# Kernel tuning notes

Measured on AMD Instinct MI355X. Metric: run time of the kernel, lower is better.

The kernel has to match this reference:

```python
import jax, jax.numpy as jnp
import numpy as np

E = 200_000   # edges (messages)
T = 2_000_000 # triplets
N = 20_000    # atoms/nodes
H = 128       # hidden_channels
INT = 64      # int_emb_size
BAS = 8       # basis_emb_size
OUT_EMB = 256 # out_emb_channels
NRAD = 6
SBF_DIM = 7 * 6  # num_spherical * num_radial = 42
NB = 4        # num_blocks
OUTC = 1      # num_targets


def setup_inputs() -> dict:
    key = jax.random.key(0)
    ks = iter(jax.random.split(key, 64))

    def w(shape):
        # glorot-ish scaled weights, stored as [in, out] for x @ W
        return jax.random.normal(next(ks), shape, jnp.float32) / np.sqrt(shape[-2])

    return dict(
        x=jax.random.normal(next(ks), (E, H), jnp.float32),
        rbf=jax.random.normal(next(ks), (E, NRAD), jnp.float32),
        sbf=jax.random.normal(next(ks), (T, SBF_DIM), jnp.float32),
        # interaction block params, stacked over NB blocks
        W_rbf1=w((NB, NRAD, BAS)), W_rbf2=w((NB, BAS, H)),
        W_sbf1=w((NB, SBF_DIM, BAS)), W_sbf2=w((NB, BAS, INT)),
        W_kj=w((NB, H, H)), b_kj=jnp.zeros((NB, H), jnp.float32),
        W_ji=w((NB, H, H)), b_ji=jnp.zeros((NB, H), jnp.float32),
        W_down=w((NB, H, INT)), W_up=w((NB, INT, H)),
        Wb=w((NB, 2, H, H)), bb=jnp.zeros((NB, 2, H), jnp.float32),   # num_before_skip=1 -> 2 linears
        Wa=w((NB, 4, H, H)), ba=jnp.zeros((NB, 4, H), jnp.float32),   # num_after_skip=2 -> 4 linears
        W_lin=w((NB, H, H)), b_lin=jnp.zeros((NB, H), jnp.float32),
        # output block params, stacked over NB+1 blocks
        Wo_rbf=w((NB + 1, NRAD, H)),
        Wo_up=w((NB + 1, H, OUT_EMB)), bo_up=jnp.zeros((NB + 1, OUT_EMB), jnp.float32),
        Wo_lins=w((NB + 1, 3, OUT_EMB, OUT_EMB)), bo_lins=jnp.zeros((NB + 1, 3, OUT_EMB), jnp.float32),
        Wo_out=w((NB + 1, OUT_EMB, OUTC)),
        idx_kj=jax.random.randint(next(ks), (T,), 0, E, jnp.int32),
        idx_ji=jax.random.randint(next(ks), (T,), 0, E, jnp.int32),
        idx_i=jax.random.randint(next(ks), (E,), 0, N, jnp.int32),
        num_nodes=N,
    )


def _interaction(b, x, rbf, sbf, idx_kj, idx_ji, p):
    act = jax.nn.silu
    x_ji = act(x @ p['W_ji'][b] + p['b_ji'][b])
    x_kj = act(x @ p['W_kj'][b] + p['b_kj'][b])
    rbf_t = (rbf @ p['W_rbf1'][b]) @ p['W_rbf2'][b]          # [E,H]
    x_kj = act((x_kj * rbf_t) @ p['W_down'][b])              # [E,INT]
    sbf_t = (sbf @ p['W_sbf1'][b]) @ p['W_sbf2'][b]          # [T,INT]
    m = x_kj[idx_kj] * sbf_t                                  # triplet gather [T,INT]
    agg = jax.ops.segment_sum(m, idx_ji, num_segments=x.shape[0])  # scatter-add [E,INT]
    x_kj = act(agg @ p['W_up'][b])                            # [E,H]
    h = x_ji + x_kj
    # residual layers before skip (1 layer = 2 linears)
    h = h + act(act(h @ p['Wb'][b, 0] + p['bb'][b, 0]) @ p['Wb'][b, 1] + p['bb'][b, 1])
    h = act(h @ p['W_lin'][b] + p['b_lin'][b]) + x
    # residual layers after skip (2 layers = 4 linears)
    for l in range(2):
        h = h + act(act(h @ p['Wa'][b, 2 * l] + p['ba'][b, 2 * l]) @ p['Wa'][b, 2 * l + 1] + p['ba'][b, 2 * l + 1])
    return h


def _output(b, x, rbf, idx_i, num_nodes, p):
    act = jax.nn.silu
    t = (rbf @ p['Wo_rbf'][b]) * x                            # [E,H]
    t = jax.ops.segment_sum(t, idx_i, num_segments=num_nodes) # [N,H]
    t = t @ p['Wo_up'][b] + p['bo_up'][b]
    for l in range(3):
        t = act(t @ p['Wo_lins'][b, l] + p['bo_lins'][b, l])
    return t @ p['Wo_out'][b]                                 # [N,OUTC]


def reference(x, rbf, sbf, W_rbf1, W_rbf2, W_sbf1, W_sbf2, W_kj, b_kj, W_ji, b_ji,
              W_down, W_up, Wb, bb, Wa, ba, W_lin, b_lin,
              Wo_rbf, Wo_up, bo_up, Wo_lins, bo_lins, Wo_out,
              idx_kj, idx_ji, idx_i, num_nodes):
    p = dict(W_rbf1=W_rbf1, W_rbf2=W_rbf2, W_sbf1=W_sbf1, W_sbf2=W_sbf2,
             W_kj=W_kj, b_kj=b_kj, W_ji=W_ji, b_ji=b_ji, W_down=W_down, W_up=W_up,
             Wb=Wb, bb=bb, Wa=Wa, ba=ba, W_lin=W_lin, b_lin=b_lin,
             Wo_rbf=Wo_rbf, Wo_up=Wo_up, bo_up=bo_up,
             Wo_lins=Wo_lins, bo_lins=bo_lins, Wo_out=Wo_out)
    P = _output(0, x, rbf, idx_i, num_nodes, p)
    for b in range(NB):  # fixed small layer loop
        x = _interaction(b, x, rbf, sbf, idx_kj, idx_ji, p)
        P = P + _output(b + 1, x, rbf, idx_i, num_nodes, p)
    return P
```

## Files before the change

### kernel.cpp

```cpp
#include <hip/hip_runtime.h>
#include <hip/hip_bf16.h>

#define E_EDGES 200000
#define T_TRIP  2000000
#define N_NODES 20000
#define H_DIM   128
#define INT_DIM 64
#define BAS     8
#define OUT_EMB 256
#define NRAD    6
#define SBF_D   42
#define NB      4

#define F_BIAS 1
#define F_SILU 2
#define F_RES  4
#define F_GATE 8

typedef __attribute__((ext_vector_type(8))) __bf16 bf16x8;
typedef __attribute__((ext_vector_type(4))) float f32x4;
typedef unsigned short u16;

__device__ __forceinline__ float silu_f(float v) { return v / (1.0f + __expf(-v)); }

__device__ __forceinline__ u16 f2bf(float f) {
    unsigned int u = __float_as_uint(f);
    u += 0x7FFF + ((u >> 16) & 1);
    return (u16)(u >> 16);
}
__device__ __forceinline__ float bf2f(u16 h) {
    return __uint_as_float(((unsigned int)h) << 16);
}

__device__ __forceinline__ void st_split(char* H, char* L, int row, int col, int stride, float v) {
    u16 hh = f2bf(v);
    u16 ll = f2bf(v - bf2f(hh));
    int off = (row * stride + col * 2) ^ ((row & 7) << 4);
    *reinterpret_cast<u16*>(H + off) = hh;
    *reinterpret_cast<u16*>(L + off) = ll;
}
__device__ __forceinline__ float ld_split(const char* H, const char* L, int row, int col, int stride) {
    int off = (row * stride + col * 2) ^ ((row & 7) << 4);
    return bf2f(*reinterpret_cast<const u16*>(H + off))
         + bf2f(*reinterpret_cast<const u16*>(L + off));
}

struct BF8x4 { bf16x8 h[4]; bf16x8 l[4]; };

__device__ __forceinline__ BF8x4 loadB128f(const u16* __restrict__ Bh, const u16* __restrict__ Bl,
                                           int k0, int wn, int l15, int khalf)
{
    BF8x4 f;
    #pragma unroll
    for (int n = 0; n < 4; ++n) {
        size_t bo = (size_t)(wn * 64 + n * 16 + l15) * 128 + k0 + khalf;
        f.h[n] = *reinterpret_cast<const bf16x8*>(Bh + bo);
        f.l[n] = *reinterpret_cast<const bf16x8*>(Bl + bo);
    }
    return f;
}
__device__ __forceinline__ BF8x4 loadB64f(const u16* __restrict__ Bh, const u16* __restrict__ Bl,
                                          int k0, int wn, int l15, int khalf)
{
    BF8x4 f;
    #pragma unroll
    for (int n = 0; n < 4; ++n) {
        size_t bo = (size_t)(wn * 64 + n * 16 + l15) * 64 + k0 + khalf;
        f.h[n] = *reinterpret_cast<const bf16x8*>(Bh + bo);
        f.l[n] = *reinterpret_cast<const bf16x8*>(Bl + bo);
    }
    return f;
}

__device__ __forceinline__ void mfma_cluster(
    const char* AH, const char* AL, int k0, int wm, int l15, int khalf,
    const BF8x4& b, f32x4 acc[2][4])
{
    #pragma unroll
    for (int m = 0; m < 2; ++m) {
        int row = wm * 32 + m * 16 + l15;
        int off = (row * 256 + (k0 + khalf) * 2) ^ ((row & 7) << 4);
        bf16x8 ah = *reinterpret_cast<const bf16x8*>(AH + off);
        bf16x8 al = *reinterpret_cast<const bf16x8*>(AL + off);
        #pragma unroll
        for (int n = 0; n < 4; ++n) {
            acc[m][n] = __builtin_amdgcn_mfma_f32_16x16x32_bf16(ah, b.h[n], acc[m][n], 0, 0, 0);
            acc[m][n] = __builtin_amdgcn_mfma_f32_16x16x32_bf16(al, b.h[n], acc[m][n], 0, 0, 0);
            acc[m][n] = __builtin_amdgcn_mfma_f32_16x16x32_bf16(ah, b.l[n], acc[m][n], 0, 0, 0);
        }
    }
}
__device__ __forceinline__ void mfma_cluster64(
    const char* AH, const char* AL, int k0, int wm, int l15, int khalf,
    const BF8x4& b, f32x4 acc[2][4])
{
    #pragma unroll
    for (int m = 0; m < 2; ++m) {
        int row = wm * 32 + m * 16 + l15;
        int off = (row * 128 + (k0 + khalf) * 2) ^ ((row & 7) << 4);
        bf16x8 ah = *reinterpret_cast<const bf16x8*>(AH + off);
        bf16x8 al = *reinterpret_cast<const bf16x8*>(AL + off);
        #pragma unroll
        for (int n = 0; n < 4; ++n) {
            acc[m][n] = __builtin_amdgcn_mfma_f32_16x16x32_bf16(ah, b.h[n], acc[m][n], 0, 0, 0);
            acc[m][n] = __builtin_amdgcn_mfma_f32_16x16x32_bf16(al, b.h[n], acc[m][n], 0, 0, 0);
            acc[m][n] = __builtin_amdgcn_mfma_f32_16x16x32_bf16(ah, b.l[n], acc[m][n], 0, 0, 0);
        }
    }
}

__device__ __forceinline__ void mm128_pipe(
    const char* AH, const char* AL,
    const u16* __restrict__ Bh, const u16* __restrict__ Bl, BF8x4& pre,
    const u16* __restrict__ nBh, const u16* __restrict__ nBl,
    int wm, int wn, int l15, int khalf, f32x4 acc[2][4])
{
    BF8x4 c0 = pre;
    BF8x4 c1 = loadB128f(Bh, Bl, 32, wn, l15, khalf);
    mfma_cluster(AH, AL, 0, wm, l15, khalf, c0, acc);
    BF8x4 c2 = loadB128f(Bh, Bl, 64, wn, l15, khalf);
    mfma_cluster(AH, AL, 32, wm, l15, khalf, c1, acc);
    BF8x4 c3 = loadB128f(Bh, Bl, 96, wn, l15, khalf);
    mfma_cluster(AH, AL, 64, wm, l15, khalf, c2, acc);
    if (nBh) pre = loadB128f(nBh, nBl, 0, wn, l15, khalf);
    mfma_cluster(AH, AL, 96, wm, l15, khalf, c3, acc);
}
__device__ __forceinline__ void mm64_pipe(
    const char* AH, const char* AL,
    const u16* __restrict__ Bh, const u16* __restrict__ Bl, BF8x4& pre,
    const u16* __restrict__ nBh, const u16* __restrict__ nBl,
    int wm, int wn, int l15, int khalf, f32x4 acc[2][4])
{
    BF8x4 c0 = pre;
    BF8x4 c1 = loadB64f(Bh, Bl, 32, wn, l15, khalf);
    mfma_cluster64(AH, AL, 0, wm, l15, khalf, c0, acc);
    if (nBh) pre = loadB128f(nBh, nBl, 0, wn, l15, khalf);
    mfma_cluster64(AH, AL, 32, wm, l15, khalf, c1, acc);
}

__global__ __launch_bounds__(256) void wprep(
    const float* __restrict__ src, u16* __restrict__ hi,
    u16* __restrict__ lo, int K, int N)
{
    int e = blockIdx.x * 256 + threadIdx.x;
    int total = K * N;
    if (e >= total) return;
    size_t base = (size_t)blockIdx.y * total;
    float a = src[base + e];
    int k = e / N, n = e - k * N;
    u16 h = f2bf(a);
    u16 l = f2bf(a - bf2f(h));
    hi[base + (size_t)n * K + k] = h;
    lo[base + (size_t)n * K + k] = l;
}

__global__ __launch_bounds__(256) void mfma_gemm(
    const float* __restrict__ A,
    const u16* __restrict__ Bhi, const u16* __restrict__ Blo,
    const float* __restrict__ bias, const float* __restrict__ res,
    const float* __restrict__ rbf8v, const float* __restrict__ Wr2,
    float* __restrict__ C, int M, int N, int K, int flags)
{
    __shared__ u16 AsH[128 * 32];
    __shared__ u16 AsL[128 * 32];

    const int tid  = threadIdx.x;
    const int lane = tid & 63;
    const int w    = tid >> 6;
    const int wm   = w >> 1, wn = w & 1;
    const int bm   = blockIdx.y * 128;
    const int bn   = blockIdx.x * 64;
    const int l15  = lane & 15;
    const int khalf = (lane >> 4) * 8;

    const int sr = tid >> 1;
    const int sc = (tid & 1) * 16;
    int grow = bm + sr; if (grow >= M) grow = M - 1;
    const float* gA = &A[(size_t)grow * K + sc];

    int bcol[2];
    #pragma unroll
    for (int n = 0; n < 2; ++n) bcol[n] = bn + wn * 32 + n * 16 + l15;

    f32x4 acc[4][2] = {};

    for (int k0 = 0; k0 < K; k0 += 32) {
        __syncthreads();
        {
            const float* p = gA + k0;
            float4 f0 = *reinterpret_cast<const float4*>(p);
            float4 f1 = *reinterpret_cast<const float4*>(p + 4);
            float4 f2 = *reinterpret_cast<const float4*>(p + 8);
            float4 f3 = *reinterpret_cast<const float4*>(p + 12);
            float vv[16] = {f0.x,f0.y,f0.z,f0.w, f1.x,f1.y,f1.z,f1.w,
                            f2.x,f2.y,f2.z,f2.w, f3.x,f3.y,f3.z,f3.w};
            const int swz = (sr & 7) << 4;
            #pragma unroll
            for (int q = 0; q < 4; ++q) {
                u16 h[4], l[4];
                #pragma unroll
                for (int j = 0; j < 4; ++j) {
                    float a = vv[q * 4 + j];
                    h[j] = f2bf(a);
                    l[j] = f2bf(a - bf2f(h[j]));
                }
                int off = (sr * 64 + (sc / 4 + q) * 8) ^ swz;
                *reinterpret_cast<ushort4*>((char*)AsH + off) = make_ushort4(h[0], h[1], h[2], h[3]);
                *reinterpret_cast<ushort4*>((char*)AsL + off) = make_ushort4(l[0], l[1], l[2], l[3]);
            }
        }
        __syncthreads();

        bf16x8 bh[2], bl[2];
        #pragma unroll
        for (int n = 0; n < 2; ++n) {
            size_t bo = (size_t)bcol[n] * K + k0 + khalf;
            bh[n] = *reinterpret_cast<const bf16x8*>(Bhi + bo);
            bl[n] = *reinterpret_cast<const bf16x8*>(Blo + bo);
        }

        #pragma unroll
        for (int m = 0; m < 4; ++m) {
            int ri  = wm * 64 + m * 16 + l15;
            int off = (ri * 64 + khalf * 2) ^ ((ri & 7) << 4);
            bf16x8 ah = *reinterpret_cast<const bf16x8*>((const char*)AsH + off);
            bf16x8 al = *reinterpret_cast<const bf16x8*>((const char*)AsL + off);
            #pragma unroll
            for (int n = 0; n < 2; ++n) {
                acc[m][n] = __builtin_amdgcn_mfma_f32_16x16x32_bf16(ah, bh[n], acc[m][n], 0, 0, 0);
                acc[m][n] = __builtin_amdgcn_mfma_f32_16x16x32_bf16(al, bh[n], acc[m][n], 0, 0, 0);
                acc[m][n] = __builtin_amdgcn_mfma_f32_16x16x32_bf16(ah, bl[n], acc[m][n], 0, 0, 0);
            }
        }
    }

    const int r4 = (lane >> 4) * 4;
    #pragma unroll
    for (int m = 0; m < 4; ++m) {
        #pragma unroll
        for (int r = 0; r < 4; ++r) {
            int row = bm + wm * 64 + m * 16 + r4 + r;
            if (row >= M) continue;
            #pragma unroll
            for (int n = 0; n < 2; ++n) {
                int col = bn + wn * 32 + n * 16 + l15;
                float v = acc[m][n][r];
                if (flags & F_BIAS) v += bias[col];
                if (flags & F_SILU) v = silu_f(v);
                if (flags & F_GATE) {
                    float g = 0.f;
                    #pragma unroll
                    for (int j = 0; j < 8; ++j)
                        g = fmaf(rbf8v[(size_t)row * 8 + j], Wr2[j * N + col], g);
                    v *= g;
                }
                if (flags & F_RES) v += res[(size_t)row * N + col];
                C[(size_t)row * N + col] = v;
            }
        }
    }
}

__global__ __launch_bounds__(256, 2) void pre_fuse(
    const float* __restrict__ X, const float* __restrict__ R8,
    const u16* __restrict__ Wjih, const u16* __restrict__ Wjil, const float* __restrict__ bji,
    const u16* __restrict__ Wkjh, const u16* __restrict__ Wkjl, const float* __restrict__ bkj,
    const float* __restrict__ Wr2,
    const u16* __restrict__ Wdnh, const u16* __restrict__ Wdnl,
    float* __restrict__ E1, float* __restrict__ C1)
{
    __shared__ u16 XH[64 * 128], XL[64 * 128];
    __shared__ u16 IH[64 * 128], IL[64 * 128];

    const int tid  = threadIdx.x;
    const int lane = tid & 63;
    const int w    = tid >> 6;
    const int wm   = w >> 1, wn = w & 1;
    const int bm   = blockIdx.x * 64;
    const int l15  = lane & 15;
    const int khalf = (lane >> 4) * 8;
    const int r4   = (lane >> 4) * 4;

    BF8x4 pre = loadB128f(Wjih, Wjil, 0, wn, l15, khalf);

    {
        int r  = tid >> 2;
        int c0 = (tid & 3) * 32;
        const float* p = &X[(size_t)(bm + r) * H_DIM + c0];
        const int swz = (r & 7) << 4;
        #pragma unroll
        for (int q = 0; q < 8; ++q) {
            float4 f = *reinterpret_cast<const float4*>(p + q * 4);
            float vv[4] = {f.x, f.y, f.z, f.w};
            u16 h[4], l[4];
            #pragma unroll
            for (int j = 0; j < 4; ++j) {
                h[j] = f2bf(vv[j]);
                l[j] = f2bf(vv[j] - bf2f(h[j]));
            }
            int off = (r * 256 + c0 * 2 + q * 8) ^ swz;
            *reinterpret_cast<ushort4*>((char*)XH + off) = make_ushort4(h[0], h[1], h[2], h[3]);
            *reinterpret_cast<ushort4*>((char*)XL + off) = make_ushort4(l[0], l[1], l[2], l[3]);
        }
    }
    __syncthreads();

    {
        f32x4 acc[2][4] = {};
        mm128_pipe((char*)XH, (char*)XL, Wjih, Wjil, pre, Wkjh, Wkjl,
                   wm, wn, l15, khalf, acc);
        #pragma unroll
        for (int n = 0; n < 4; ++n) {
            int col = wn * 64 + n * 16 + l15;
            float bv = bji[col];
            #pragma unroll
            for (int m = 0; m < 2; ++m)
                #pragma unroll
                for (int r = 0; r < 4; ++r) {
                    int row = wm * 32 + m * 16 + r4 + r;
                    E1[(size_t)(bm + row) * H_DIM + col] = silu_f(acc[m][n][r] + bv);
                }
        }
    }
    {
        f32x4 acc[2][4] = {};
        mm128_pipe((char*)XH, (char*)XL, Wkjh, Wkjl, pre, nullptr, nullptr,
                   wm, wn, l15, khalf, acc);
        #pragma unroll
        for (int n = 0; n < 4; ++n) {
            int col = wn * 64 + n * 16 + l15;
            float bv = bkj[col];
            #pragma unroll
            for (int m = 0; m < 2; ++m)
                #pragma unroll
                for (int r = 0; r < 4; ++r) {
                    int row = wm * 32 + m * 16 + r4 + r;
                    float v = silu_f(acc[m][n][r] + bv);
                    float g = 0.f;
                    #pragma unroll
                    for (int j = 0; j < 8; ++j)
                        g = fmaf(R8[(size_t)(bm + row) * 8 + j], Wr2[j * H_DIM + col], g);
                    st_split((char*)IH, (char*)IL, row, col, 256, v * g);
                }
        }
    }
    __syncthreads();

    {
        f32x4 acc[2][2] = {};
        #pragma unroll
        for (int k0 = 0; k0 < 128; k0 += 32) {
            bf16x8 bh[2], bl[2];
            #pragma unroll
            for (int n = 0; n < 2; ++n) {
                size_t bo = (size_t)(wn * 32 + n * 16 + l15) * 128 + k0 + khalf;
                bh[n] = *reinterpret_cast<const bf16x8*>(Wdnh + bo);
                bl[n] = *reinterpret_cast<const bf16x8*>(Wdnl + bo);
            }
            #pragma unroll
            for (int m = 0; m < 2; ++m) {
                int row = wm * 32 + m * 16 + l15;
                int off = (row * 256 + (k0 + khalf) * 2) ^ ((row & 7) << 4);
                bf16x8 ah = *reinterpret_cast<const bf16x8*>((const char*)IH + off);
                bf16x8 al = *reinterpret_cast<const bf16x8*>((const char*)IL + off);
                #pragma unroll
                for (int n = 0; n < 2; ++n) {
                    acc[m][n] = __builtin_amdgcn_mfma_f32_16x16x32_bf16(ah, bh[n], acc[m][n], 0, 0, 0);
                    acc[m][n] = __builtin_amdgcn_mfma_f32_16x16x32_bf16(al, bh[n], acc[m][n], 0, 0, 0);
                    acc[m][n] = __builtin_amdgcn_mfma_f32_16x16x32_bf16(ah, bl[n], acc[m][n], 0, 0, 0);
                }
            }
        }
        #pragma unroll
        for (int n = 0; n < 2; ++n) {
            int col = wn * 32 + n * 16 + l15;
            #pragma unroll
            for (int m = 0; m < 2; ++m)
                #pragma unroll
                for (int r = 0; r < 4; ++r) {
                    int row = wm * 32 + m * 16 + r4 + r;
                    C1[(size_t)(bm + row) * INT_DIM + col] = silu_f(acc[m][n][r]);
                }
        }
    }
}

struct ChainP {
    const u16 *uph, *upl;
    const u16 *b0h, *b0l, *b1h, *b1l;
    const u16 *lnh, *lnl;
    const u16 *a0h, *a0l, *a1h, *a1l, *a2h, *a2l, *a3h, *a3l;
    const float *bb0, *bb1, *blin, *ba0, *ba1, *ba2, *ba3;
};

__global__ __launch_bounds__(256, 2) void post_chain(
    const float* __restrict__ AGG, const float* __restrict__ E1,
    const float* __restrict__ X, ChainP p, float* __restrict__ OUT)
{
    __shared__ u16 GH[64 * 64],  GL[64 * 64];
    __shared__ u16 P0H[64 * 128], P0L[64 * 128];
    __shared__ u16 P1H[64 * 128], P1L[64 * 128];

    const int tid  = threadIdx.x;
    const int lane = tid & 63;
    const int w    = tid >> 6;
    const int wm   = w >> 1, wn = w & 1;
    const int bm   = blockIdx.x * 64;
    const int l15  = lane & 15;
    const int khalf = (lane >> 4) * 8;
    const int r4   = (lane >> 4) * 4;

    BF8x4 pre = loadB64f(p.uph, p.upl, 0, wn, l15, khalf);

    {
        int r  = tid >> 2;
        int c0 = (tid & 3) * 16;
        const float* pg = &AGG[(size_t)(bm + r) * INT_DIM + c0];
        const int swz = (r & 7) << 4;
        #pragma unroll
        for (int q = 0; q < 4; ++q) {
            float4 f = *reinterpret_cast<const float4*>(pg + q * 4);
            float vv[4] = {f.x, f.y, f.z, f.w};
            u16 h[4], l[4];
            #pragma unroll
            for (int j = 0; j < 4; ++j) {
                h[j] = f2bf(vv[j]);
                l[j] = f2bf(vv[j] - bf2f(h[j]));
            }
            int off = (r * 128 + c0 * 2 + q * 8) ^ swz;
            *reinterpret_cast<ushort4*>((char*)GH + off) = make_ushort4(h[0], h[1], h[2], h[3]);
            *reinterpret_cast<ushort4*>((char*)GL + off) = make_ushort4(l[0], l[1], l[2], l[3]);
        }
    }
    __syncthreads();

    f32x4 acc[2][4];

    #pragma unroll
    for (int m = 0; m < 2; ++m)
        #pragma unroll
        for (int n = 0; n < 4; ++n) acc[m][n] = f32x4{0.f, 0.f, 0.f, 0.f};
    mm64_pipe((char*)GH, (char*)GL, p.uph, p.upl, pre, p.b0h, p.b0l,
              wm, wn, l15, khalf, acc);
    #pragma unroll
    for (int n = 0; n < 4; ++n) {
        int col = wn * 64 + n * 16 + l15;
        #pragma unroll
        for (int m = 0; m < 2; ++m)
            #pragma unroll
            for (int r = 0; r < 4; ++r) {
                int row = wm * 32 + m * 16 + r4 + r;
                float v = E1[(size_t)(bm + row) * H_DIM + col] + silu_f(acc[m][n][r]);
                st_split((char*)P0H, (char*)P0L, row, col, 256, v);
            }
// ... 25 lines not shown
    }

    #define STAGE_RES(SRC_H, SRC_L, WH, WL, BIAS, RES_H, RES_L, NWH, NWL)               \
    {                                                                                   \
        _Pragma("unroll")                                                               \
        for (int m = 0; m < 2; ++m)                                                     \
            _Pragma("unroll")                                                           \
            for (int n = 0; n < 4; ++n) acc[m][n] = f32x4{0.f, 0.f, 0.f, 0.f};          \
        mm128_pipe((char*)SRC_H, (char*)SRC_L, WH, WL, pre, NWH, NWL,                   \
                   wm, wn, l15, khalf, acc);                                            \
        _Pragma("unroll")                                                               \
        for (int n = 0; n < 4; ++n) {                                                   \
            int col = wn * 64 + n * 16 + l15;                                           \
            float bv = BIAS[col];                                                       \
            _Pragma("unroll")                                                           \
            for (int m = 0; m < 2; ++m)                                                 \
                _Pragma("unroll")                                                       \
                for (int r = 0; r < 4; ++r) {                                           \
                    int row = wm * 32 + m * 16 + r4 + r;                                \
                    float v = ld_split((char*)RES_H, (char*)RES_L, row, col, 256)       \
                            + silu_f(acc[m][n][r] + bv);                                \
                    st_split((char*)RES_H, (char*)RES_L, row, col, 256, v);             \
                }                                                                       \
        }                                                                               \
        __syncthreads();                                                                \
    }

    STAGE_PLAIN(P0H, P0L, p.b0h, p.b0l, p.bb0, P1H, P1L, p.b1h, p.b1l)
    STAGE_RES(P1H, P1L, p.b1h, p.b1l, p.bb1, P0H, P0L, p.lnh, p.lnl)

    {
        #pragma unroll
        for (int m = 0; m < 2; ++m)
            #pragma unroll
            for (int n = 0; n < 4; ++n) acc[m][n] = f32x4{0.f, 0.f, 0.f, 0.f};
        mm128_pipe((char*)P0H, (char*)P0L, p.lnh, p.lnl, pre, p.a0h, p.a0l,
                   wm, wn, l15, khalf, acc);
        #pragma unroll
        for (int n = 0; n < 4; ++n) {
            int col = wn * 64 + n * 16 + l15;
            float bv = p.blin[col];
            #pragma unroll
            for (int m = 0; m < 2; ++m)
                #pragma unroll
                for (int r = 0; r < 4; ++r) {
                    int row = wm * 32 + m * 16 + r4 + r;
                    float v = silu_f(acc[m][n][r] + bv) + X[(size_t)(bm + row) * H_DIM + col];
                    st_split((char*)P1H, (char*)P1L, row, col, 256, v);
                }
        }
        __syncthreads();
    }

    STAGE_PLAIN(P1H, P1L, p.a0h, p.a0l, p.ba0, P0H, P0L, p.a1h, p.a1l)
    STAGE_RES(P0H, P0L, p.a1h, p.a1l, p.ba1, P1H, P1L, p.a2h, p.a2l)
    STAGE_PLAIN(P1H, P1L, p.a2h, p.a2l, p.ba2, P0H, P0L, p.a3h, p.a3l)

    {
        #pragma unroll
        for (int m = 0; m < 2; ++m)
            #pragma unroll
            for (int n = 0; n < 4; ++n) acc[m][n] = f32x4{0.f, 0.f, 0.f, 0.f};
        mm128_pipe((char*)P0H, (char*)P0L, p.a3h, p.a3l, pre, nullptr, nullptr,
                   wm, wn, l15, khalf, acc);
        #pragma unroll
        for (int n = 0; n < 4; ++n) {
            int col = wn * 64 + n * 16 + l15;
            float bv = p.ba3[col];
            #pragma unroll
            for (int m = 0; m < 2; ++m)
                #pragma unroll
                for (int r = 0; r < 4; ++r) {
                    int row = wm * 32 + m * 16 + r4 + r;
                    float v = ld_split((char*)P1H, (char*)P1L, row, col, 256)
                            + silu_f(acc[m][n][r] + bv);
                    OUT[(size_t)(bm + row) * H_DIM + col] = v;
                }
        }
    }
    #undef STAGE_PLAIN
    #undef STAGE_RES
}

__global__ __launch_bounds__(256) void rbf8_kernel(
    const float* __restrict__ rbf, const float* __restrict__ W1,
    float* __restrict__ r8, int Ecount)
{
    int e = blockIdx.x * blockDim.x + threadIdx.x;
    if (e >= Ecount) return;
    float rv[NRAD];
    #pragma unroll
    for (int k = 0; k < NRAD; ++k) rv[k] = rbf[(size_t)e * NRAD + k];
    float acc[BAS] = {};
    #pragma unroll
    for (int k = 0; k < NRAD; ++k)
        #pragma unroll
        for (int j = 0; j < BAS; ++j)
            acc[j] = fmaf(rv[k], W1[k * BAS + j], acc[j]);
    float4* o = reinterpret_cast<float4*>(&r8[(size_t)e * BAS]);
    o[0] = make_float4(acc[0], acc[1], acc[2], acc[3]);
    o[1] = make_float4(acc[4], acc[5], acc[6], acc[7]);
}

__global__ __launch_bounds__(256) void csr_count(
    const int* __restrict__ idx, int* __restrict__ cnt, int n)
{
    int i = blockIdx.x * 256 + threadIdx.x;
    if (i < n) atomicAdd(&cnt[idx[i]], 1);
}

__global__ __launch_bounds__(256) void scan_block(
    const int* __restrict__ cnt, int* __restrict__ ptr, int* __restrict__ bsum, int n)
{
    __shared__ int s[256];
    int i = blockIdx.x * 256 + threadIdx.x;
    int v = (i < n) ? cnt[i] : 0;
    s[threadIdx.x] = v;
    __syncthreads();
    #pragma unroll
    for (int off = 1; off < 256; off <<= 1) {
        int t = (threadIdx.x >= off) ? s[threadIdx.x - off] : 0;
        __syncthreads();
        s[threadIdx.x] += t;
        __syncthreads();
    }
    if (i < n) ptr[i] = s[threadIdx.x] - v;
    if (threadIdx.x == 255) bsum[blockIdx.x] = s[255];
}

__global__ __launch_bounds__(1024) void scan_aux(int* __restrict__ bsum, int nb)
{
    __shared__ int s[1024];
    int v = (threadIdx.x < nb) ? bsum[threadIdx.x] : 0;
    s[threadIdx.x] = v;
    __syncthreads();
    #pragma unroll
    for (int off = 1; off < 1024; off <<= 1) {
        int t = (threadIdx.x >= off) ? s[threadIdx.x - off] : 0;
        __syncthreads();
        s[threadIdx.x] += t;
        __syncthreads();
    }
    if (threadIdx.x < nb) bsum[threadIdx.x] = s[threadIdx.x] - v;
}

__global__ __launch_bounds__(256) void scan_add(
    int* __restrict__ ptr, const int* __restrict__ bsum, int n)
{
    int i = blockIdx.x * 256 + threadIdx.x;
    if (i < n) ptr[i] += bsum[blockIdx.x];
}

__global__ __launch_bounds__(256) void csr_fill(
    const int* __restrict__ idx, int* __restrict__ cursor,
    int* __restrict__ perm, int n)
{
    int i = blockIdx.x * 256 + threadIdx.x;
    if (i >= n) return;
    int pos = atomicAdd(&cursor[idx[i]], 1);
    perm[pos] = i;
}

__global__ __launch_bounds__(256) void permute_s8(
    const float* __restrict__ sbf, const float* __restrict__ W1all,
    const int* __restrict__ idx_kj, const int* __restrict__ tperm,
    u16* __restrict__ ps8, int* __restrict__ pkj, int Tcount)
// ... 30 lines not shown
        *reinterpret_cast<ushort4*>(op) = o0;
        *reinterpret_cast<ushort4*>(op + 4) = o1;
    }
}

__device__ __forceinline__ float dot8_bf(uint4 r, const float* w2) {
    float s;
    s  = bf2f((u16)(r.x)) * w2[0] + bf2f((u16)(r.x >> 16)) * w2[1];
    s += bf2f((u16)(r.y)) * w2[2] + bf2f((u16)(r.y >> 16)) * w2[3];
    s += bf2f((u16)(r.z)) * w2[4] + bf2f((u16)(r.z >> 16)) * w2[5];
    s += bf2f((u16)(r.w)) * w2[6] + bf2f((u16)(r.w >> 16)) * w2[7];
    return s;
}

__global__ __launch_bounds__(256) void triplet_gather2(
    const u16* __restrict__ ps8b, const float* __restrict__ Wsb2,
    const float* __restrict__ xkj, const int* __restrict__ pkj,
    const int* __restrict__ tptr, const int* __restrict__ tcnt,
    float* __restrict__ agg, int Ecount)
{
    const int lane = threadIdx.x & 63;
    int wid = (blockIdx.x * blockDim.x + threadIdx.x) >> 6;
    const int nw = (gridDim.x * blockDim.x) >> 6;
    float w2[BAS];
    #pragma unroll
    for (int j = 0; j < BAS; ++j) w2[j] = Wsb2[j * INT_DIM + lane];

    for (int e = wid; e < Ecount; e += nw) {
        int start = tptr[e];
        int end   = start + tcnt[e];
        float acc0 = 0.f, acc1 = 0.f;
        int i = start;
        for (; i + 1 < end; i += 2) {
            uint4 ra = *reinterpret_cast<const uint4*>(&ps8b[(size_t)i * BAS]);
            uint4 rb = *reinterpret_cast<const uint4*>(&ps8b[(size_t)(i + 1) * BAS]);
            int e0 = pkj[i], e1 = pkj[i + 1];
            float s0 = dot8_bf(ra, w2);
            float s1 = dot8_bf(rb, w2);
            acc0 = fmaf(xkj[(size_t)e0 * INT_DIM + lane], s0, acc0);
            acc1 = fmaf(xkj[(size_t)e1 * INT_DIM + lane], s1, acc1);
        }
        if (i < end) {
            uint4 ra = *reinterpret_cast<const uint4*>(&ps8b[(size_t)i * BAS]);
            int e0 = pkj[i];
            acc0 = fmaf(xkj[(size_t)e0 * INT_DIM + lane], dot8_bf(ra, w2), acc0);
        }
        agg[(size_t)e * INT_DIM + lane] = acc0 + acc1;
    }
}

__global__ __launch_bounds__(256) void out_gather(
    const float* __restrict__ rbf, const float* __restrict__ Wor,
    const float* __restrict__ x,
    const int* __restrict__ eptr, const int* __restrict__ ecnt,
    const int* __restrict__ eperm, float* __restrict__ tN, int Nn)
{
    const int lane = threadIdx.x & 63;
    int wid = (blockIdx.x * blockDim.x + threadIdx.x) >> 6;
    const int nw = (gridDim.x * blockDim.x) >> 6;
    float wr0[NRAD], wr1[NRAD];
    #pragma unroll
    for (int k = 0; k < NRAD; ++k) {
        wr0[k] = Wor[k * H_DIM + lane];
        wr1[k] = Wor[k * H_DIM + lane + 64];
    }
    for (int n = wid; n < Nn; n += nw) {
        int start = eptr[n];
        int end   = start + ecnt[n];
        float a0 = 0.f, a1 = 0.f;
        for (int i = start; i < end; ++i) {
            int e = eperm[i];
            const float2* rp = reinterpret_cast<const float2*>(&rbf[(size_t)e * NRAD]);
            float2 r0 = rp[0], r1 = rp[1], r2 = rp[2];
            float rA = r0.x*wr0[0] + r0.y*wr0[1] + r1.x*wr0[2]
                     + r1.y*wr0[3] + r2.x*wr0[4] + r2.y*wr0[5];
            float rB = r0.x*wr1[0] + r0.y*wr1[1] + r1.x*wr1[2]
                     + r1.y*wr1[3] + r2.x*wr1[4] + r2.y*wr1[5];
            a0 = fmaf(rA, x[(size_t)e * H_DIM + lane], a0);
            a1 = fmaf(rB, x[(size_t)e * H_DIM + lane + 64], a1);
        }
        tN[(size_t)n * H_DIM + lane] = a0;
        tN[(size_t)n * H_DIM + lane + 64] = a1;
    }
}

__global__ __launch_bounds__(256) void out_final(
    const float* __restrict__ Tb, const float* __restrict__ Wo,
    float* __restrict__ P, int Nn)
{
    const int lane = threadIdx.x & 63;
    int node = (blockIdx.x * blockDim.x + threadIdx.x) >> 6;
    if (node >= Nn) return;
    float s = 0.f;
    #pragma unroll
    for (int i = 0; i < 4; ++i) {
        int c = lane + i * 64;
        s = fmaf(Tb[(size_t)node * OUT_EMB + c], Wo[c], s);
    }
    #pragma unroll
    for (int o = 32; o > 0; o >>= 1) s += __shfl_xor(s, o);
    if (lane == 0) P[node] += s;
}

extern "C" void kernel_launch(void* const* d_in, const int* in_sizes, int n_in,
                              void* d_out, int out_size, void* d_ws, size_t ws_size,
                              hipStream_t stream)
{
    const float* x_in    = (const float*)d_in[0];
    const float* rbf     = (const float*)d_in[1];
    const float* sbf     = (const float*)d_in[2];
    const float* W_rbf1  = (const float*)d_in[3];
    const float* W_rbf2  = (const float*)d_in[4];
    const float* W_sbf1  = (const float*)d_in[5];
    const float* W_sbf2  = (const float*)d_in[6];
    const float* W_kj    = (const float*)d_in[7];
    const float* b_kj    = (const float*)d_in[8];
    const float* W_ji    = (const float*)d_in[9];
    const float* b_ji    = (const float*)d_in[10];
    const float* W_down  = (const float*)d_in[11];
    const float* W_up    = (const float*)d_in[12];
    const float* Wb      = (const float*)d_in[13];
    const float* bb      = (const float*)d_in[14];
    const float* Wa      = (const float*)d_in[15];
    const float* ba      = (const float*)d_in[16];
    const float* W_lin   = (const float*)d_in[17];
    const float* b_lin   = (const float*)d_in[18];
    const float* Wo_rbf  = (const float*)d_in[19];
    const float* Wo_up   = (const float*)d_in[20];
    const float* bo_up   = (const float*)d_in[21];
    const float* Wo_lins = (const float*)d_in[22];
    const float* bo_lins = (const float*)d_in[23];
    const float* Wo_out  = (const float*)d_in[24];
    const int*   idx_kj  = (const int*)d_in[25];
    const int*   idx_ji  = (const int*)d_in[26];
    const int*   idx_i   = (const int*)d_in[27];

    char* ws = (char*)d_ws;
    size_t off = 0;
    auto alloc = [&](size_t bytes) -> void* {
        void* p = (void*)(ws + off);
        off += (bytes + 255) & ~(size_t)255;
        return p;
    };
    float* XA = (float*)alloc((size_t)E_EDGES * H_DIM * 4);
    float* XB = (float*)alloc((size_t)E_EDGES * H_DIM * 4);
    float* E1 = (float*)alloc((size_t)E_EDGES * H_DIM * 4);
    float* C1 = (float*)alloc((size_t)E_EDGES * INT_DIM * 4);
    float* C2 = (float*)alloc((size_t)E_EDGES * INT_DIM * 4);
    float* R8 = (float*)alloc((size_t)E_EDGES * BAS * 4);
    float* TN = (float*)alloc((size_t)N_NODES * H_DIM * 4);
    float* T1 = (float*)alloc((size_t)N_NODES * OUT_EMB * 4);
    float* T2 = (float*)alloc((size_t)N_NODES * OUT_EMB * 4);
    u16* HKJ = (u16*)alloc(4  * 16384 * 2); u16* LKJ = (u16*)alloc(4  * 16384 * 2);
    u16* HJI = (u16*)alloc(4  * 16384 * 2); u16* LJI = (u16*)alloc(4  * 16384 * 2);
    u16* HDN = (u16*)alloc(4  * 8192  * 2); u16* LDN = (u16*)alloc(4  * 8192  * 2);
    u16* HUP = (u16*)alloc(4  * 8192  * 2); u16* LUP = (u16*)alloc(4  * 8192  * 2);
    u16* HWB = (u16*)alloc(8  * 16384 * 2); u16* LWB = (u16*)alloc(8  * 16384 * 2);
    u16* HWA = (u16*)alloc(16 * 16384 * 2); u16* LWA = (u16*)alloc(16 * 16384 * 2);
    u16* HLN = (u16*)alloc(4  * 16384 * 2); u16* LLN = (u16*)alloc(4  * 16384 * 2);
    u16* HOU = (u16*)alloc(5  * 32768 * 2); u16* LOU = (u16*)alloc(5  * 32768 * 2);
    u16* HOL = (u16*)alloc(15 * 65536 * 2); u16* LOL = (u16*)alloc(15 * 65536 * 2);
    int* tcnt  = (int*)alloc((size_t)E_EDGES * 4);
    int* tptr  = (int*)alloc((size_t)E_EDGES * 4);
    int* tcur  = (int*)alloc((size_t)E_EDGES * 4);
    int* tperm = (int*)alloc((size_t)T_TRIP * 4);
    int* tbsum = (int*)alloc(1024 * 4);
    int* ecnt  = (int*)alloc((size_t)N_NODES * 4);
    int* eptr  = (int*)alloc((size_t)N_NODES * 4);
    int* ecur  = (int*)alloc((size_t)N_NODES * 4);
    int* eperm = (int*)alloc((size_t)E_EDGES * 4);
    int* ebsum = (int*)alloc(1024 * 4);
    u16* PS8 = (u16*)alloc((size_t)NB * T_TRIP * BAS * 2);
    int* PKJ = (int*)alloc((size_t)T_TRIP * 4);
    (void)ws_size;

    auto prep = [&](const float* src, u16* hi, u16* lo, int K, int N, int cnt) {
        dim3 g((K * N + 255) / 256, cnt);
        hipLaunchKernelGGL(wprep, g, dim3(256), 0, stream, src, hi, lo, K, N);
    };
    prep(W_kj,    HKJ, LKJ, 128, 128, 4);
    prep(W_ji,    HJI, LJI, 128, 128, 4);
    prep(W_down,  HDN, LDN, 128, 64,  4);
    prep(W_up,    HUP, LUP, 64,  128, 4);
    prep(Wb,      HWB, LWB, 128, 128, 8);
    prep(Wa,      HWA, LWA, 128, 128, 16);
    prep(W_lin,   HLN, LLN, 128, 128, 4);
    prep(Wo_up,   HOU, LOU, 128, 256, 5);
    prep(Wo_lins, HOL, LOL, 256, 256, 15);

    {
        const int nbT = (E_EDGES + 255) / 256;
        hipMemsetAsync(tcnt, 0, (size_t)E_EDGES * 4, stream);
        hipLaunchKernelGGL(csr_count, dim3((T_TRIP + 255) / 256), dim3(256), 0, stream,
                           idx_ji, tcnt, T_TRIP);
        hipLaunchKernelGGL(scan_block, dim3(nbT), dim3(256), 0, stream, tcnt, tptr, tbsum, E_EDGES);
        hipLaunchKernelGGL(scan_aux, dim3(1), dim3(1024), 0, stream, tbsum, nbT);
        hipLaunchKernelGGL(scan_add, dim3(nbT), dim3(256), 0, stream, tptr, tbsum, E_EDGES);
        hipMemcpyAsync(tcur, tptr, (size_t)E_EDGES * 4, hipMemcpyDeviceToDevice, stream);
        hipLaunchKernelGGL(csr_fill, dim3((T_TRIP + 255) / 256), dim3(256), 0, stream,
                           idx_ji, tcur, tperm, T_TRIP);
    }
    {
        const int nbN = (N_NODES + 255) / 256;
        hipMemsetAsync(ecnt, 0, (size_t)N_NODES * 4, stream);
        hipLaunchKernelGGL(csr_count, dim3((E_EDGES + 255) / 256), dim3(256), 0, stream,
                           idx_i, ecnt, E_EDGES);
        hipLaunchKernelGGL(scan_block, dim3(nbN), dim3(256), 0, stream, ecnt, eptr, ebsum, N_NODES);
        hipLaunchKernelGGL(scan_aux, dim3(1), dim3(1024), 0, stream, ebsum, nbN);
        hipLaunchKernelGGL(scan_add, dim3(nbN), dim3(256), 0, stream, eptr, ebsum, N_NODES);
        hipMemcpyAsync(ecur, eptr, (size_t)N_NODES * 4, hipMemcpyDeviceToDevice, stream);
        hipLaunchKernelGGL(csr_fill, dim3((E_EDGES + 255) / 256), dim3(256), 0, stream,
                           idx_i, ecur, eperm, E_EDGES);
    }
    hipLaunchKernelGGL(permute_s8, dim3((T_TRIP + 255) / 256), dim3(256), 0, stream,
                       sbf, W_sbf1, idx_kj, tperm, PS8, PKJ, T_TRIP);

    auto gemm = [&](const float* A, const u16* Bh, const u16* Bl, const float* bias,
                    const float* res, const float* r8, const float* Wr2f,
                    float* C, int M, int N, int K, int flags) {
        dim3 g(N / 64, (M + 127) / 128), b(256);
        hipLaunchKernelGGL(mfma_gemm, g, b, 0, stream,
                           A, Bh, Bl, bias, res, r8, Wr2f, C, M, N, K, flags);
    };

    float* P = (float*)d_out;
    hipMemsetAsync(P, 0, (size_t)N_NODES * sizeof(float), stream);

    auto out_block = [&](int ob, const float* xcur) {
        hipLaunchKernelGGL(out_gather, dim3(2048), dim3(256), 0, stream,
                           rbf, Wo_rbf + (size_t)ob * NRAD * H_DIM, xcur,
                           eptr, ecnt, eperm, TN, N_NODES);
        gemm(TN, HOU + (size_t)ob * 32768, LOU + (size_t)ob * 32768,
             bo_up + (size_t)ob * OUT_EMB, nullptr, nullptr, nullptr,
             T1, N_NODES, OUT_EMB, H_DIM, F_BIAS);
        float* src = T1; float* dst = T2;
        for (int l = 0; l < 3; ++l) {
            gemm(src, HOL + (size_t)(ob * 3 + l) * 65536, LOL + (size_t)(ob * 3 + l) * 65536,
                 bo_lins + (size_t)(ob * 3 + l) * OUT_EMB, nullptr, nullptr, nullptr,
                 dst, N_NODES, OUT_EMB, OUT_EMB, F_BIAS | F_SILU);
            float* tmp = src; src = dst; dst = tmp;
        }
        hipLaunchKernelGGL(out_final, dim3((N_NODES * 64 + 255) / 256), dim3(256), 0, stream,
                           src, Wo_out + (size_t)ob * OUT_EMB, P, N_NODES);
    };

    out_block(0, x_in);

    const float* xcur = x_in;
    const int EB = E_EDGES / 64;
    for (int b = 0; b < NB; ++b) {
        float* xnext = (b % 2 == 0) ? XB : XA;
        hipLaunchKernelGGL(rbf8_kernel, dim3((E_EDGES + 255) / 256), dim3(256), 0, stream,
                           rbf, W_rbf1 + (size_t)b * NRAD * BAS, R8, E_EDGES);
        hipLaunchKernelGGL(pre_fuse, dim3(EB), dim3(256), 0, stream,
                           xcur, R8,
                           HJI + (size_t)b * 16384, LJI + (size_t)b * 16384, b_ji + (size_t)b * H_DIM,
                           HKJ + (size_t)b * 16384, LKJ + (size_t)b * 16384, b_kj + (size_t)b * H_DIM,
                           W_rbf2 + (size_t)b * BAS * H_DIM,
                           HDN + (size_t)b * 8192, LDN + (size_t)b * 8192,
                           E1, C1);
        hipLaunchKernelGGL(triplet_gather2, dim3(2048), dim3(256), 0, stream,
                           PS8 + (size_t)b * T_TRIP * BAS, W_sbf2 + (size_t)b * BAS * INT_DIM,
                           C1, PKJ, tptr, tcnt, C2, E_EDGES);
        ChainP cp;
        cp.uph = HUP + (size_t)b * 8192;  cp.upl = LUP + (size_t)b * 8192;
        cp.b0h = HWB + (size_t)(b * 2 + 0) * 16384; cp.b0l = LWB + (size_t)(b * 2 + 0) * 16384;
        cp.b1h = HWB + (size_t)(b * 2 + 1) * 16384; cp.b1l = LWB + (size_t)(b * 2 + 1) * 16384;
        cp.lnh = HLN + (size_t)b * 16384; cp.lnl = LLN + (size_t)b * 16384;
        cp.a0h = HWA + (size_t)(b * 4 + 0) * 16384; cp.a0l = LWA + (size_t)(b * 4 + 0) * 16384;
        cp.a1h = HWA + (size_t)(b * 4 + 1) * 16384; cp.a1l = LWA + (size_t)(b * 4 + 1) * 16384;
        cp.a2h = HWA + (size_t)(b * 4 + 2) * 16384; cp.a2l = LWA + (size_t)(b * 4 + 2) * 16384;
        cp.a3h = HWA + (size_t)(b * 4 + 3) * 16384; cp.a3l = LWA + (size_t)(b * 4 + 3) * 16384;
        cp.bb0 = bb + (size_t)(b * 2 + 0) * H_DIM;
        cp.bb1 = bb + (size_t)(b * 2 + 1) * H_DIM;
        cp.blin = b_lin + (size_t)b * H_DIM;
        cp.ba0 = ba + (size_t)(b * 4 + 0) * H_DIM;
        cp.ba1 = ba + (size_t)(b * 4 + 1) * H_DIM;
        cp.ba2 = ba + (size_t)(b * 4 + 2) * H_DIM;
        cp.ba3 = ba + (size_t)(b * 4 + 3) * H_DIM;
        hipLaunchKernelGGL(post_chain, dim3(EB), dim3(256), 0, stream,
                           C2, E1, xcur, cp, xnext);
        xcur = xnext;
        out_block(b + 1, xcur);
    }
}
```

Baseline: 4.618 ms.

## Fuse output-block MLP chain into one kernel with LDS-resident intermediates

Replaces the four separate GEMM launches and the final reduction of each output block with a single out_chain kernel. Each block keeps 32 node rows resident in shared memory as split bf16 hi/lo values across the up-projection, three SiLU linears and the final dot product. This removes the global round-trips of the N×256 intermediates and several launches. It also wraps the MFMA clusters in s_setprio to raise wave priority during matrix math. The cost is large LDS use per block, which limits occupancy, and each block re-reads the full weight matrices from global memory or cache.

Measured after the change: 4.438 ms. -3.9%, faster.

```diff
diff --git a/kernel.cpp b/kernel.cpp
--- a/kernel.cpp
+++ b/kernel.cpp
@@ -12,11 +12,6 @@
 #define SBF_D   42
 #define NB      4
 
-#define F_BIAS 1
-#define F_SILU 2
-#define F_RES  4
-#define F_GATE 8
-
 typedef __attribute__((ext_vector_type(8))) __bf16 bf16x8;
 typedef __attribute__((ext_vector_type(4))) float f32x4;
 typedef unsigned short u16;
@@ -71,11 +66,24 @@
     }
     return f;
 }
+__device__ __forceinline__ BF8x4 loadB256f(const u16* __restrict__ Bh, const u16* __restrict__ Bl,
+                                           int k0, int wn, int l15, int khalf)
+{
+    BF8x4 f;
+    #pragma unroll
+    for (int n = 0; n < 4; ++n) {
+        size_t bo = (size_t)(wn * 64 + n * 16 + l15) * 256 + k0 + khalf;
+        f.h[n] = *reinterpret_cast<const bf16x8*>(Bh + bo);
+        f.l[n] = *reinterpret_cast<const bf16x8*>(Bl + bo);
+    }
+    return f;
+}
 
 __device__ __forceinline__ void mfma_cluster(
     const char* AH, const char* AL, int k0, int wm, int l15, int khalf,
     const BF8x4& b, f32x4 acc[2][4])
 {
+    __builtin_amdgcn_s_setprio(1);
     #pragma unroll
     for (int m = 0; m < 2; ++m) {
         int row = wm * 32 + m * 16 + l15;
@@ -89,11 +97,13 @@
             acc[m][n] = __builtin_amdgcn_mfma_f32_16x16x32_bf16(ah, b.l[n], acc[m][n], 0, 0, 0);
         }
     }
+    __builtin_amdgcn_s_setprio(0);
 }
 __device__ __forceinline__ void mfma_cluster64(
     const char* AH, const char* AL, int k0, int wm, int l15, int khalf,
     const BF8x4& b, f32x4 acc[2][4])
 {
+    __builtin_amdgcn_s_setprio(1);
     #pragma unroll
     for (int m = 0; m < 2; ++m) {
         int row = wm * 32 + m * 16 + l15;
@@ -107,6 +117,27 @@
             acc[m][n] = __builtin_amdgcn_mfma_f32_16x16x32_bf16(ah, b.l[n], acc[m][n], 0, 0, 0);
         }
     }
+    __builtin_amdgcn_s_setprio(0);
+}
+__device__ __forceinline__ void mfma_cluster512(
+    const char* AH, const char* AL, int k0, int l15, int khalf,
+    const BF8x4& b, f32x4 acc[2][4])
+{
+    __builtin_amdgcn_s_setprio(1);
+    #pragma unroll
+    for (int m = 0; m < 2; ++m) {
+        int row = m * 16 + l15;
+        int off = (row * 512 + (k0 + khalf) * 2) ^ ((row & 7) << 4);
+        bf16x8 ah = *reinterpret_cast<const bf16x8*>(AH + off);
+        bf16x8 al = *reinterpret_cast<const bf16x8*>(AL + off);
+        #pragma unroll
+        for (int n = 0; n < 4; ++n) {
+            acc[m][n] = __builtin_amdgcn_mfma_f32_16x16x32_bf16(ah, b.h[n], acc[m][n], 0, 0, 0);
+            acc[m][n] = __builtin_amdgcn_mfma_f32_16x16x32_bf16(al, b.h[n], acc[m][n], 0, 0, 0);
+            acc[m][n] = __builtin_amdgcn_mfma_f32_16x16x32_bf16(ah, b.l[n], acc[m][n], 0, 0, 0);
+        }
+    }
+    __builtin_amdgcn_s_setprio(0);
 }
 
 __device__ __forceinline__ void mm128_pipe(
@@ -152,113 +183,6 @@
     u16 l = f2bf(a - bf2f(h));
     hi[base + (size_t)n * K + k] = h;
     lo[base + (size_t)n * K + k] = l;
-}
-
-__global__ __launch_bounds__(256) void mfma_gemm(
-    const float* __restrict__ A,
-    const u16* __restrict__ Bhi, const u16* __restrict__ Blo,
-    const float* __restrict__ bias, const float* __restrict__ res,
-    const float* __restrict__ rbf8v, const float* __restrict__ Wr2,
-    float* __restrict__ C, int M, int N, int K, int flags)
-{
-    __shared__ u16 AsH[128 * 32];
-    __shared__ u16 AsL[128 * 32];
-
-    const int tid  = threadIdx.x;
-    const int lane = tid & 63;
-    const int w    = tid >> 6;
-    const int wm   = w >> 1, wn = w & 1;
-    const int bm   = blockIdx.y * 128;
-    const int bn   = blockIdx.x * 64;
-    const int l15  = lane & 15;
-    const int khalf = (lane >> 4) * 8;
-
-    const int sr = tid >> 1;
-    const int sc = (tid & 1) * 16;
-    int grow = bm + sr; if (grow >= M) grow = M - 1;
-    const float* gA = &A[(size_t)grow * K + sc];
-
-    int bcol[2];
-    #pragma unroll
-    for (int n = 0; n < 2; ++n) bcol[n] = bn + wn * 32 + n * 16 + l15;
-
-    f32x4 acc[4][2] = {};
-
-    for (int k0 = 0; k0 < K; k0 += 32) {
-        __syncthreads();
-        {
-            const float* p = gA + k0;
-            float4 f0 = *reinterpret_cast<const float4*>(p);
-            float4 f1 = *reinterpret_cast<const float4*>(p + 4);
-            float4 f2 = *reinterpret_cast<const float4*>(p + 8);
-            float4 f3 = *reinterpret_cast<const float4*>(p + 12);
-            float vv[16] = {f0.x,f0.y,f0.z,f0.w, f1.x,f1.y,f1.z,f1.w,
-                            f2.x,f2.y,f2.z,f2.w, f3.x,f3.y,f3.z,f3.w};
-            const int swz = (sr & 7) << 4;
-            #pragma unroll
-            for (int q = 0; q < 4; ++q) {
-                u16 h[4], l[4];
-                #pragma unroll
-                for (int j = 0; j < 4; ++j) {
-                    float a = vv[q * 4 + j];
-                    h[j] = f2bf(a);
-                    l[j] = f2bf(a - bf2f(h[j]));
-                }
-                int off = (sr * 64 + (sc / 4 + q) * 8) ^ swz;
-                *reinterpret_cast<ushort4*>((char*)AsH + off) = make_ushort4(h[0], h[1], h[2], h[3]);
-                *reinterpret_cast<ushort4*>((char*)AsL + off) = make_ushort4(l[0], l[1], l[2], l[3]);
-            }
-        }
-        __syncthreads();
-
-        bf16x8 bh[2], bl[2];
-        #pragma unroll
-        for (int n = 0; n < 2; ++n) {
-            size_t bo = (size_t)bcol[n] * K + k0 + khalf;
-            bh[n] = *reinterpret_cast<const bf16x8*>(Bhi + bo);
-            bl[n] = *reinterpret_cast<const bf16x8*>(Blo + bo);
-        }
-
-        #pragma unroll
-        for (int m = 0; m < 4; ++m) {
-            int ri  = wm * 64 + m * 16 + l15;
-            int off = (ri * 64 + khalf * 2) ^ ((ri & 7) << 4);
-            bf16x8 ah = *reinterpret_cast<const bf16x8*>((const char*)AsH + off);
-            bf16x8 al = *reinterpret_cast<const bf16x8*>((const char*)AsL + off);
-            #pragma unroll
-            for (int n = 0; n < 2; ++n) {
-                acc[m][n] = __builtin_amdgcn_mfma_f32_16x16x32_bf16(ah, bh[n], acc[m][n], 0, 0, 0);
-                acc[m][n] = __builtin_amdgcn_mfma_f32_16x16x32_bf16(al, bh[n], acc[m][n], 0, 0, 0);
-                acc[m][n] = __builtin_amdgcn_mfma_f32_16x16x32_bf16(ah, bl[n], acc[m][n], 0, 0, 0);
-            }
-        }
-    }
-
-    const int r4 = (lane >> 4) * 4;
-    #pragma unroll
-    for (int m = 0; m < 4; ++m) {
-        #pragma unroll
-        for (int r = 0; r < 4; ++r) {
-            int row = bm + wm * 64 + m * 16 + r4 + r;
-            if (row >= M) continue;
-            #pragma unroll
-            for (int n = 0; n < 2; ++n) {
-                int col = bn + wn * 32 + n * 16 + l15;
-                float v = acc[m][n][r];
-                if (flags & F_BIAS) v += bias[col];
-                if (flags & F_SILU) v = silu_f(v);
-                if (flags & F_GATE) {
-                    float g = 0.f;
-                    #pragma unroll
-                    for (int j = 0; j < 8; ++j)
-                        g = fmaf(rbf8v[(size_t)row * 8 + j], Wr2[j * N + col], g);
-                    v *= g;
-                }
-                if (flags & F_RES) v += res[(size_t)row * N + col];
-                C[(size_t)row * N + col] = v;
-            }
-        }
-    }
 }
 
 __global__ __launch_bounds__(256, 2) void pre_fuse(
@@ -357,6 +281,7 @@
                 bh[n] = *reinterpret_cast<const bf16x8*>(Wdnh + bo);
                 bl[n] = *reinterpret_cast<const bf16x8*>(Wdnl + bo);
             }
+            __builtin_amdgcn_s_setprio(1);
             #pragma unroll
             for (int m = 0; m < 2; ++m) {
                 int row = wm * 32 + m * 16 + l15;
@@ -370,6 +295,7 @@
                     acc[m][n] = __builtin_amdgcn_mfma_f32_16x16x32_bf16(ah, bl[n], acc[m][n], 0, 0, 0);
                 }
             }
+            __builtin_amdgcn_s_setprio(0);
         }
         #pragma unroll
         for (int n = 0; n < 2; ++n) {
@@ -561,6 +487,128 @@
     #undef STAGE_RES
 }
 
+__global__ __launch_bounds__(256, 2) void out_chain(
+    const float* __restrict__ TN,
+    const u16* __restrict__ Uh, const u16* __restrict__ Ul, const float* __restrict__ bu,
+    const u16* __restrict__ L0h, const u16* __restrict__ L0l, const float* __restrict__ b0,
+    const u16* __restrict__ L1h, const u16* __restrict__ L1l, const float* __restrict__ b1,
+    const u16* __restrict__ L2h, const u16* __restrict__ L2l, const float* __restrict__ b2,
+    const float* __restrict__ Wo, float* __restrict__ P)
+{
+    __shared__ u16 XH[32 * 128], XL[32 * 128];
+    __shared__ u16 T0H[32 * 256], T0L[32 * 256];
+    __shared__ u16 T1H[32 * 256], T1L[32 * 256];
+
+    const int tid  = threadIdx.x;
+    const int lane = tid & 63;
+    const int wn   = tid >> 6;
+    const int bm   = blockIdx.x * 32;
+    const int l15  = lane & 15;
+    const int khalf = (lane >> 4) * 8;
+    const int r4   = (lane >> 4) * 4;
+
+    {
+        int r  = tid >> 3;
+        int c0 = (tid & 7) * 16;
+        const float* p = &TN[(size_t)(bm + r) * H_DIM + c0];
+        const int swz = (r & 7) << 4;
+        #pragma unroll
+        for (int q = 0; q < 4; ++q) {
+            float4 f = *reinterpret_cast<const float4*>(p + q * 4);
+            float vv[4] = {f.x, f.y, f.z, f.w};
+            u16 h[4], l[4];
+            #pragma unroll
+            for (int j = 0; j < 4; ++j) {
+                h[j] = f2bf(vv[j]);
+                l[j] = f2bf(vv[j] - bf2f(h[j]));
+            }
+            int off = (r * 256 + c0 * 2 + q * 8) ^ swz;
+            *reinterpret_cast<ushort4*>((char*)XH + off) = make_ushort4(h[0], h[1], h[2], h[3]);
+            *reinterpret_cast<ushort4*>((char*)XL + off) = make_ushort4(l[0], l[1], l[2], l[3]);
+        }
+    }
+    __syncthreads();
+
+    f32x4 acc[2][4];
+
+    {
+        #pragma unroll
+        for (int m = 0; m < 2; ++m)
+            #pragma unroll
+            for (int n = 0; n < 4; ++n) acc[m][n] = f32x4{0.f, 0.f, 0.f, 0.f};
+        BF8x4 cur = loadB128f(Uh, Ul, 0, wn, l15, khalf);
+        #pragma unroll
+        for (int k = 0; k < 4; ++k) {
+            BF8x4 nxt;
+            if (k < 3) nxt = loadB128f(Uh, Ul, 32 * (k + 1), wn, l15, khalf);
+            mfma_cluster((char*)XH, (char*)XL, 32 * k, 0, l15, khalf, cur, acc);
+            if (k < 3) cur = nxt;
+        }
+        #pragma unroll
+        for (int n = 0; n < 4; ++n) {
+            int col = wn * 64 + n * 16 + l15;
+            float bv = bu[col];
+            #pragma unroll
+            for (int m = 0; m < 2; ++m)
+                #pragma unroll
+                for (int r = 0; r < 4; ++r) {
+                    int row = m * 16 + r4 + r;
+                    st_split((char*)T0H, (char*)T0L, row, col, 512, acc[m][n][r] + bv);
+                }
+        }
+        __syncthreads();
+    }
+
+    #define OLIN(SRC_H, SRC_L, WH, WL, BIAS, DST_H, DST_L)                              \
+    {                                                                                   \
+        _Pragma("unroll")                                                               \
+        for (int m = 0; m < 2; ++m)                                                     \
+            _Pragma("unroll")                                                           \
+            for (int n = 0; n < 4; ++n) acc[m][n] = f32x4{0.f, 0.f, 0.f, 0.f};          \
+        BF8x4 cur = loadB256f(WH, WL, 0, wn, l15, khalf);                               \
+        _Pragma("unroll")                                                               \
+        for (int k = 0; k < 8; ++k) {                                                   \
+            BF8x4 nxt;                                                                  \
+            if (k < 7) nxt = loadB256f(WH, WL, 32 * (k + 1), wn, l15, khalf);           \
+            mfma_cluster512((char*)SRC_H, (char*)SRC_L, 32 * k, l15, khalf, cur, acc);  \
+            if (k < 7) cur = nxt;                                                       \
+        }                                                                               \
+        _Pragma("unroll")                                                               \
+        for (int n = 0; n < 4; ++n) {                                                   \
+            int col = wn * 64 + n * 16 + l15;                                           \
+            float bv = BIAS[col];                                                       \
+            _Pragma("unroll")                                                           \
+            for (int m = 0; m < 2; ++m)                                                 \
+                _Pragma("unroll")                                                       \
+                for (int r = 0; r < 4; ++r) {                                           \
+                    int row = m * 16 + r4 + r;                                          \
+                    st_split((char*)DST_H, (char*)DST_L, row, col, 512,                 \
+                             silu_f(acc[m][n][r] + bv));                                \
+                }                                                                       \
+        }                                                                               \
+        __syncthreads();                                                                \
+    }
+
+    OLIN(T0H, T0L, L0h, L0l, b0, T1H, T1L)
+    OLIN(T1H, T1L, L1h, L1l, b1, T0H, T0L)
+    OLIN(T0H, T0L, L2h, L2l, b2, T1H, T1L)
+    #undef OLIN
+
+    {
+        int row  = tid >> 3;
+        int part = tid & 7;
+        float s = 0.f;
+        int cbase = part * 32;
+        #pragma unroll
+        for (int c = 0; c < 32; ++c)
+            s = fmaf(ld_split((char*)T1H, (char*)T1L, row, cbase + c, 512), Wo[cbase + c], s);
+        s += __shfl_xor(s, 1);
+        s += __shfl_xor(s, 2);
+        s += __shfl_xor(s, 4);
+        if (part == 0) P[bm + row] += s;
+    }
+}
+
 __global__ __launch_bounds__(256) void rbf8_kernel(
     const float* __restrict__ rbf, const float* __restrict__ W1,
     float* __restrict__ r8, int Ecount)
@@ -757,24 +805,6 @@
         tN[(size_t)n * H_DIM + lane] = a0;
         tN[(size_t)n * H_DIM + lane + 64] = a1;
     }
-}
-
-__global__ __launch_bounds__(256) void out_final(
-    const float* __restrict__ Tb, const float* __restrict__ Wo,
-    float* __restrict__ P, int Nn)
-{
-    const int lane = threadIdx.x & 63;
-    int node = (blockIdx.x * blockDim.x + threadIdx.x) >> 6;
-    if (node >= Nn) return;
-    float s = 0.f;
-    #pragma unroll
-    for (int i = 0; i < 4; ++i) {
-        int c = lane + i * 64;
-        s = fmaf(Tb[(size_t)node * OUT_EMB + c], Wo[c], s);
-    }
-    #pragma unroll
-    for (int o = 32; o > 0; o >>= 1) s += __shfl_xor(s, o);
-    if (lane == 0) P[node] += s;
 }
 
 extern "C" void kernel_launch(void* const* d_in, const int* in_sizes, int n_in,
@@ -824,8 +854,6 @@
     float* C2 = (float*)alloc((size_t)E_EDGES * INT_DIM * 4);
     float* R8 = (float*)alloc((size_t)E_EDGES * BAS * 4);
     float* TN = (float*)alloc((size_t)N_NODES * H_DIM * 4);
-    float* T1 = (float*)alloc((size_t)N_NODES * OUT_EMB * 4);
-    float* T2 = (float*)alloc((size_t)N_NODES * OUT_EMB * 4);
     u16* HKJ = (u16*)alloc(4  * 16384 * 2); u16* LKJ = (u16*)alloc(4  * 16384 * 2);
     u16* HJI = (u16*)alloc(4  * 16384 * 2); u16* LJI = (u16*)alloc(4  * 16384 * 2);
     u16* HDN = (u16*)alloc(4  * 8192  * 2); u16* LDN = (u16*)alloc(4  * 8192  * 2);
@@ -890,14 +918,6 @@
     hipLaunchKernelGGL(permute_s8, dim3((T_TRIP + 255) / 256), dim3(256), 0, stream,
                        sbf, W_sbf1, idx_kj, tperm, PS8, PKJ, T_TRIP);
 
-    auto gemm = [&](const float* A, const u16* Bh, const u16* Bl, const float* bias,
-                    const float* res, const float* r8, const float* Wr2f,
-                    float* C, int M, int N, int K, int flags) {
-        dim3 g(N / 64, (M + 127) / 128), b(256);
-        hipLaunchKernelGGL(mfma_gemm, g, b, 0, stream,
-                           A, Bh, Bl, bias, res, r8, Wr2f, C, M, N, K, flags);
-    };
-
     float* P = (float*)d_out;
     hipMemsetAsync(P, 0, (size_t)N_NODES * sizeof(float), stream);
 
@@ -905,18 +925,17 @@
         hipLaunchKernelGGL(out_gather, dim3(2048), dim3(256), 0, stream,
                            rbf, Wo_rbf + (size_t)ob * NRAD * H_DIM, xcur,
                            eptr, ecnt, eperm, TN, N_NODES);
-        gemm(TN, HOU + (size_t)ob * 32768, LOU + (size_t)ob * 32768,
-             bo_up + (size_t)ob * OUT_EMB, nullptr, nullptr, nullptr,
-             T1, N_NODES, OUT_EMB, H_DIM, F_BIAS);
-        float* src = T1; float* dst = T2;
-        for (int l = 0; l < 3; ++l) {
-            gemm(src, HOL + (size_t)(ob * 3 + l) * 65536, LOL + (size_t)(ob * 3 + l) * 65536,
-                 bo_lins + (size_t)(ob * 3 + l) * OUT_EMB, nullptr, nullptr, nullptr,
-                 dst, N_NODES, OUT_EMB, OUT_EMB, F_BIAS | F_SILU);
-            float* tmp = src; src = dst; dst = tmp;
-        }
-        hipLaunchKernelGGL(out_final, dim3((N_NODES * 64 + 255) / 256), dim3(256), 0, stream,
-                           src, Wo_out + (size_t)ob * OUT_EMB, P, N_NODES);
+        hipLaunchKernelGGL(out_chain, dim3(N_NODES / 32), dim3(256), 0, stream,
+                           TN,
+                           HOU + (size_t)ob * 32768, LOU + (size_t)ob * 32768,
+                           bo_up + (size_t)ob * OUT_EMB,
+                           HOL + (size_t)(ob * 3 + 0) * 65536, LOL + (size_t)(ob * 3 + 0) * 65536,
+                           bo_lins + (size_t)(ob * 3 + 0) * OUT_EMB,
+                           HOL + (size_t)(ob * 3 + 1) * 65536, LOL + (size_t)(ob * 3 + 1) * 65536,
+                           bo_lins + (size_t)(ob * 3 + 1) * OUT_EMB,
+                           HOL + (size_t)(ob * 3 + 2) * 65536, LOL + (size_t)(ob * 3 + 2) * 65536,
+                           bo_lins + (size_t)(ob * 3 + 2) * OUT_EMB,
+                           Wo_out + (size_t)ob * OUT_EMB, P);
     };
 
     out_block(0, x_in);
```
